# Kernel optimization log

Measured on AMD Instinct MI355X. Metric: run time of the kernel, lower is better.

## Reference

```python
import jax, jax.numpy as jnp
import numpy as np

FRAC_BIT = 12
SCALE = float(2 ** FRAC_BIT)          # 12 fractional bits
QMIN, QMAX = -32768.0, 32767.0        # signed 16-bit two's complement range


def quant16(x):
    """Quantize to signed 16-bit fixed point with 12 fractional bits.

    Matches float_to_16bits_tensor / bit_slice semantics: the bit-serial
    crossbar MVM of the sliced operands equals an exact integer product of
    these fixed-point values, rescaled back to float.
    """
    return jnp.clip(jnp.round(x * SCALE), QMIN, QMAX) / SCALE


def setup_inputs() -> dict:
    key = jax.random.key(0)
    k1, k2 = jax.random.split(key)
    x = jax.random.normal(k1, (32, 128, 56, 56), dtype=jnp.float32)
    # kaiming-ish scale so weights are well inside the fixed-point range
    weight = jax.random.normal(k2, (256, 128, 3, 3), dtype=jnp.float32) * 0.05
    return {"x": x, "weight": weight}


def reference(x, weight):
    # The nested i/j loop in the original slides a stride-1 window over the
    # zero-padded input, performing a bit-sliced crossbar MVM per pixel.
    # That is exactly conv2d(stride=1, padding=1) on 16-bit fixed-point
    # quantized input and weight (bias row in the crossbar is zero / unused).
    qx = quant16(x)
    qw = quant16(weight)
    out = jax.lax.conv_general_dilated(
        qx, qw,
        window_strides=(1, 1),
        padding=((1, 1), (1, 1)),
        dimension_numbers=("NCHW", "OIHW", "NCHW"),
    )
    return out
```

## Files before the change

### kernel.cpp

```cpp
#include <hip/hip_runtime.h>
#include <cstdint>
#include <cstddef>


typedef __attribute__((ext_vector_type(8))) short short8;
typedef __attribute__((ext_vector_type(4))) float floatx4;

#define NIMG 32
#define CIN  128
#define HW   56
#define KOUT 256
#define HP   58
#define XPAD_ELEMS ((size_t)NIMG * HP * HP * CIN)
#define WT_OFF_BYTES (XPAD_ELEMS * 2)
#define KK 1152

__device__ __forceinline__ uint16_t quant_bf16(float v) {
    float q = rintf(v * 4096.0f);
    q = fminf(fmaxf(q, -32768.0f), 32767.0f) * (1.0f / 4096.0f);
    union { float f; uint32_t u; } cv; cv.f = q;
    uint32_t u = cv.u;
    return (uint16_t)((u + 0x7fffu + ((u >> 16) & 1u)) >> 16);
}

__global__ __launch_bounds__(256) void quant_pad_x(const float* __restrict__ x,
                                                   uint16_t* __restrict__ xp) {
    const int b = blockIdx.x;
    const int n = b / HP, hp = b - n * HP;
    uint16_t* row = xp + (size_t)(n * HP + hp) * HP * CIN;

    if (hp == 0 || hp == HP - 1) {
        uint4 z{0, 0, 0, 0};
        uint4* d = (uint4*)row;
        for (int t = threadIdx.x; t < HP * CIN * 2 / 16; t += 256) d[t] = z;
        return;
    }
    const int h = hp - 1;
    __shared__ uint16_t tile[HW * 130];
    const float* src = x + (size_t)n * CIN * HW * HW + (size_t)h * HW;
    for (int t = threadIdx.x; t < CIN * 14; t += 256) {
        int c = t / 14, w4 = t - c * 14;
        float4 v = *(const float4*)(src + (size_t)c * (HW * HW) + w4 * 4);
        int base = (w4 * 4) * 130 + c;
        tile[base]       = quant_bf16(v.x);
        tile[base + 130] = quant_bf16(v.y);
        tile[base + 260] = quant_bf16(v.z);
        tile[base + 390] = quant_bf16(v.w);
    }
    __syncthreads();
    if (threadIdx.x < 32) {
        uint4 z{0, 0, 0, 0};
        if (threadIdx.x < 16) ((uint4*)row)[threadIdx.x] = z;
        else ((uint4*)(row + 57 * CIN))[threadIdx.x - 16] = z;
    }
    uint2* dst = (uint2*)(row + CIN);
    for (int t = threadIdx.x; t < (HW * CIN) / 4; t += 256) {
        int w = t >> 5, c4 = (t & 31) * 4;
        uint32_t a = tile[w * 130 + c4]     | ((uint32_t)tile[w * 130 + c4 + 1] << 16);
        uint32_t c = tile[w * 130 + c4 + 2] | ((uint32_t)tile[w * 130 + c4 + 3] << 16);
        dst[t] = make_uint2(a, c);
    }
}

__global__ __launch_bounds__(256) void quant_w(const float* __restrict__ w,
                                               uint16_t* __restrict__ wt) {
    int i = blockIdx.x * 256 + threadIdx.x;
    int k = i / KK;
    int r = i - k * KK;
    int tap = r >> 7;
    int c = r & 127;
    wt[i] = quant_bf16(w[(size_t)(k * CIN + c) * 9 + tap]);
}


#define GLOAD(gsrc, ldst)                                                      \
    __builtin_amdgcn_global_load_lds(                                          \
        (__attribute__((address_space(1))) void*)(void*)(gsrc),                \
        (__attribute__((address_space(3))) void*)(void*)(ldst), 16, 0, 0)

#define STAGE_A(bsel, kt) do {                                                 \
    GLOAD(aGp[0][0] + (size_t)(kt) * 64, &ldsA[bsel][0][(wv * 8) * 64]);       \
    GLOAD(aGp[0][1] + (size_t)(kt) * 64, &ldsA[bsel][0][(64 + wv * 8) * 64]);  \
    GLOAD(aGp[1][0] + (size_t)(kt) * 64, &ldsA[bsel][1][(wv * 8) * 64]);       \
    GLOAD(aGp[1][1] + (size_t)(kt) * 64, &ldsA[bsel][1][(64 + wv * 8) * 64]);  \
} while (0)

#define STAGE_B(bsel, kt) do {                                                 \
    const int tap_ = (kt) >> 1;                                                \
    const size_t boff_ = (size_t)((tap_ / 3) * HP + (tap_ % 3)) * CIN          \
                       + (size_t)((kt) & 1) * 64;                              \
    GLOAD(bGp[0][0] + boff_, &ldsB[bsel][0][(wv * 8) * 64]);                   \
    GLOAD(bGp[0][1] + boff_, &ldsB[bsel][0][(64 + wv * 8) * 64]);              \
    GLOAD(bGp[1][0] + boff_, &ldsB[bsel][1][(wv * 8) * 64]);                   \
    GLOAD(bGp[1][1] + boff_, &ldsB[bsel][1][(64 + wv * 8) * 64]);              \
} while (0)

#define READ_A(bsel, q4) do {                                                  \
    _Pragma("unroll")                                                          \
    for (int f_ = 0; f_ < 4; ++f_) {                                           \
        const int r_ = (q4) * 64 + f_ * 16 + m16;                              \
        ra[f_][0] = *(const short8*)&ldsA[bsel][wm][r_ * 64 + sl0];            \
        ra[f_][1] = *(const short8*)&ldsA[bsel][wm][r_ * 64 + sl1];            \
    }                                                                          \
} while (0)

#define READ_B(dst, bsel, ch) do {                                             \
    _Pragma("unroll")                                                          \
    for (int fc_ = 0; fc_ < 2; ++fc_) {                                        \
        const int r_ = bl + (ch) * 32 + fc_ * 16 + m16;                        \
        dst[fc_][0] = *(const short8*)&ldsB[bsel][bh][r_ * 64 + sl0];          \
        dst[fc_][1] = *(const short8*)&ldsB[bsel][bh][r_ * 64 + sl1];          \
    }                                                                          \
} while (0)

#define MFMA_Q(q4, ch, B) do {                                                 \
    _Pragma("unroll")                                                          \
    for (int s_ = 0; s_ < 2; ++s_)                                             \
    _Pragma("unroll")                                                          \
    for (int f_ = 0; f_ < 4; ++f_)                                             \
    _Pragma("unroll")                                                          \
    for (int c_ = 0; c_ < 2; ++c_)                                             \
        acc[q4][f_][ch][c_] = __builtin_amdgcn_mfma_f32_16x16x32_bf16(         \
            ra[f_][s_], B[c_][s_], acc[q4][f_][ch][c_], 0, 0, 0);              \
} while (0)

#define PHASE_TAIL(...) do {                                                   \
    __builtin_amdgcn_s_barrier();                                              \
    asm volatile("s_waitcnt lgkmcnt(0)" ::: "memory");                         \
    __builtin_amdgcn_s_setprio(1);                                             \
    __VA_ARGS__;                                                               \
    __builtin_amdgcn_s_setprio(0);                                             \
    __builtin_amdgcn_s_barrier();                                              \
} while (0)

__global__ __launch_bounds__(512, 2) void conv_gemm(const uint16_t* __restrict__ xp,
                                                    const uint16_t* __restrict__ wt,
                                                    float* __restrict__ out) {
    __shared__ __align__(16) uint16_t ldsA[2][2][128 * 64];
    __shared__ __align__(16) uint16_t ldsB[2][2][128 * 64];

    const int tid  = threadIdx.x;
    const int l    = tid & 63;
    const int wv   = tid >> 6;
    const int wm   = wv >> 2;
    const int wn   = wv & 3;
    const int bh   = wn >> 1;
    const int bl   = (wn & 1) * 64;
    const int srow = l >> 3;
    const int c_data = (l & 7) ^ srow;
    const int m16  = l & 15;
    const int q    = l >> 4;
    const int r7   = m16 & 7;
    const int sl0  = ((0 + q) ^ r7) * 8;
    const int sl1  = ((4 + q) ^ r7) * 8;

    const int b = blockIdx.x;
    const int pxblk = (b & 7) * 49 + (b >> 3);

    const uint16_t* aGp[2][2];
    const uint16_t* bGp[2][2];
#pragma unroll
    for (int h_ = 0; h_ < 2; ++h_)
#pragma unroll
        for (int j_ = 0; j_ < 2; ++j_) {
            const int row = h_ * 128 + j_ * 64 + wv * 8 + srow;
            aGp[h_][j_] = wt + (size_t)row * KK + c_data * 8;
            const int p = pxblk * 256 + row;
            const int n = p / 3136; const int rem = p - n * 3136;
            const int hh = rem / HW; const int ww = rem - hh * HW;
            bGp[h_][j_] = xp + (size_t)((n * HP + hh) * HP + ww) * CIN + c_data * 8;
        }

    floatx4 acc[2][4][2][2];
#pragma unroll
    for (int a_ = 0; a_ < 2; ++a_)
#pragma unroll
        for (int f_ = 0; f_ < 4; ++f_)
#pragma unroll
            for (int c_ = 0; c_ < 2; ++c_)
#pragma unroll
                for (int d_ = 0; d_ < 2; ++d_)
                    acc[a_][f_][c_][d_] = (floatx4){0.f, 0.f, 0.f, 0.f};

    short8 ra[4][2];
    short8 rb0[2][2];
    short8 rb1[2][2];

    STAGE_A(0, 0); STAGE_B(0, 0);
    STAGE_A(1, 1); STAGE_B(1, 1);
    asm volatile("s_waitcnt vmcnt(8)" ::: "memory");
    __builtin_amdgcn_s_barrier();

#pragma unroll 1
    for (int it = 0; it < 8; ++it) {
        const int ktE = 2 * it + 2;
        const int ktO = 2 * it + 3;
        READ_A(0, 0);
        READ_B(rb0, 0, 0);
        PHASE_TAIL(MFMA_Q(0, 0, rb0));
        READ_B(rb1, 0, 1);
        PHASE_TAIL(MFMA_Q(0, 1, rb1));
        READ_A(0, 1);
        PHASE_TAIL(MFMA_Q(1, 0, rb0));
        STAGE_A(0, ktE); STAGE_B(0, ktE);
        asm volatile("s_waitcnt vmcnt(8)" ::: "memory");
        PHASE_TAIL(MFMA_Q(1, 1, rb1));
        READ_A(1, 0);
        READ_B(rb0, 1, 0);
        PHASE_TAIL(MFMA_Q(0, 0, rb0));
        READ_B(rb1, 1, 1);
        PHASE_TAIL(MFMA_Q(0, 1, rb1));
        READ_A(1, 1);
        PHASE_TAIL(MFMA_Q(1, 0, rb0));
        STAGE_A(1, ktO); STAGE_B(1, ktO);
        asm volatile("s_waitcnt vmcnt(8)" ::: "memory");
        PHASE_TAIL(MFMA_Q(1, 1, rb1));
    }

    READ_A(0, 0);
    READ_B(rb0, 0, 0);
    PHASE_TAIL(MFMA_Q(0, 0, rb0));
    READ_B(rb1, 0, 1);
    PHASE_TAIL(MFMA_Q(0, 1, rb1));
    READ_A(0, 1);
    PHASE_TAIL(MFMA_Q(1, 0, rb0));
    asm volatile("s_waitcnt vmcnt(0)" ::: "memory");
    PHASE_TAIL(MFMA_Q(1, 1, rb1));
    READ_A(1, 0);
    READ_B(rb0, 1, 0);
    PHASE_TAIL(MFMA_Q(0, 0, rb0));
    READ_B(rb1, 1, 1);
    PHASE_TAIL(MFMA_Q(0, 1, rb1));
    READ_A(1, 1);
    PHASE_TAIL(MFMA_Q(1, 0, rb0));
    PHASE_TAIL(MFMA_Q(1, 1, rb1));

#pragma unroll
    for (int ch = 0; ch < 2; ++ch) {
        const int p0 = pxblk * 256 + wn * 64 + ch * 32 + m16;
        const int n = p0 / 3136; const int rem0 = p0 - n * 3136;
        float* opb = out + (size_t)(n * KOUT + wm * 128) * 3136 + rem0;
#pragma unroll
        for (int q4 = 0; q4 < 2; ++q4)
#pragma unroll
            for (int f = 0; f < 4; ++f) {
                const int kl = q4 * 64 + f * 16 + q * 4;
#pragma unroll
                for (int t = 0; t < 4; ++t) {
                    float* op = opb + (size_t)(kl + t) * 3136;
                    op[0]  = acc[q4][f][ch][0][t];
                    op[16] = acc[q4][f][ch][1][t];
                }
            }
    }
}

extern "C" void kernel_launch(void* const* d_in, const int* in_sizes, int n_in,
                              void* d_out, int out_size, void* d_ws, size_t ws_size,
                              hipStream_t stream) {
    const float* x = (const float*)d_in[0];
    const float* w = (const float*)d_in[1];
    float* out = (float*)d_out;

    uint16_t* xp  = (uint16_t*)d_ws;
    uint16_t* wtb = (uint16_t*)((char*)d_ws + WT_OFF_BYTES);

    quant_pad_x<<<NIMG * HP, 256, 0, stream>>>(x, xp);
    quant_w<<<(KOUT * KK) / 256, 256, 0, stream>>>(w, wtb);

    conv_gemm<<<dim3(392), dim3(512), 0, stream>>>(xp, wtb, out);
}
```

Before: 217.7 us.

## Cut per-phase barriers to two per k-tile in conv GEMM main loop

Replaces the eight barrier-pair phases per iteration with one body per k-tile that reads A/B fragments and issues MFMAs with no intermediate barriers, followed by a single barrier-stage-wait-barrier block. The goal is to remove frequent workgroup barriers and explicit lgkmcnt waits that serialize the waves and stall the MFMA pipe. The trade-off is that the compiler now places LDS waits itself, and the loss of lockstep wave interleaving may raise LDS contention or register pressure.

```diff
diff --git a/kernel.cpp b/kernel.cpp
--- a/kernel.cpp
+++ b/kernel.cpp
@@ -124,12 +124,25 @@
             ra[f_][s_], B[c_][s_], acc[q4][f_][ch][c_], 0, 0, 0);              \
 } while (0)
 
-#define PHASE_TAIL(...) do {                                                   \
+#define KT_BODY(bsel) do {                                                     \
+    READ_A(bsel, 0);                                                           \
+    READ_B(rb0, bsel, 0);                                                      \
+    READ_B(rb1, bsel, 1);                                                      \
+    __builtin_amdgcn_s_setprio(1);                                             \
+    MFMA_Q(0, 0, rb0);                                                         \
+    MFMA_Q(0, 1, rb1);                                                         \
+    __builtin_amdgcn_s_setprio(0);                                             \
+    READ_A(bsel, 1);                   \
+    __builtin_amdgcn_s_setprio(1);                                             \
+    MFMA_Q(1, 0, rb0);                                                         \
+    MFMA_Q(1, 1, rb1);                                                         \
+    __builtin_amdgcn_s_setprio(0);                                             \
+} while (0)
+
+#define KT_SYNC_STAGE(bsel, ktn) do {                                          \
     __builtin_amdgcn_s_barrier();                                              \
-    asm volatile("s_waitcnt lgkmcnt(0)" ::: "memory");                         \
-    __builtin_amdgcn_s_setprio(1);                                             \
-    __VA_ARGS__;                                                               \
-    __builtin_amdgcn_s_setprio(0);                                             \
+    STAGE_A(bsel, ktn); STAGE_B(bsel, ktn);                                    \
+    asm volatile("s_waitcnt vmcnt(8)" ::: "memory");                           \
     __builtin_amdgcn_s_barrier();                                              \
 } while (0)
 
@@ -195,45 +208,17 @@
     for (int it = 0; it < 8; ++it) {
         const int ktE = 2 * it + 2;
         const int ktO = 2 * it + 3;
-        READ_A(0, 0);
-        READ_B(rb0, 0, 0);
-        PHASE_TAIL(MFMA_Q(0, 0, rb0));
-        READ_B(rb1, 0, 1);
-        PHASE_TAIL(MFMA_Q(0, 1, rb1));
-        READ_A(0, 1);
-        PHASE_TAIL(MFMA_Q(1, 0, rb0));
-        STAGE_A(0, ktE); STAGE_B(0, ktE);
-        asm volatile("s_waitcnt vmcnt(8)" ::: "memory");
-        PHASE_TAIL(MFMA_Q(1, 1, rb1));
-        READ_A(1, 0);
-        READ_B(rb0, 1, 0);
-        PHASE_TAIL(MFMA_Q(0, 0, rb0));
-        READ_B(rb1, 1, 1);
-        PHASE_TAIL(MFMA_Q(0, 1, rb1));
-        READ_A(1, 1);
-        PHASE_TAIL(MFMA_Q(1, 0, rb0));
-        STAGE_A(1, ktO); STAGE_B(1, ktO);
-        asm volatile("s_waitcnt vmcnt(8)" ::: "memory");
-        PHASE_TAIL(MFMA_Q(1, 1, rb1));
-    }
-
-    READ_A(0, 0);
-    READ_B(rb0, 0, 0);
-    PHASE_TAIL(MFMA_Q(0, 0, rb0));
-    READ_B(rb1, 0, 1);
-    PHASE_TAIL(MFMA_Q(0, 1, rb1));
-    READ_A(0, 1);
-    PHASE_TAIL(MFMA_Q(1, 0, rb0));
+        KT_BODY(0);
+        KT_SYNC_STAGE(0, ktE);
+        KT_BODY(1);
+        KT_SYNC_STAGE(1, ktO);
+    }
+
+    KT_BODY(0);
+    __builtin_amdgcn_s_barrier();
     asm volatile("s_waitcnt vmcnt(0)" ::: "memory");
-    PHASE_TAIL(MFMA_Q(1, 1, rb1));
-    READ_A(1, 0);
-    READ_B(rb0, 1, 0);
-    PHASE_TAIL(MFMA_Q(0, 0, rb0));
-    READ_B(rb1, 1, 1);
-    PHASE_TAIL(MFMA_Q(0, 1, rb1));
-    READ_A(1, 1);
-    PHASE_TAIL(MFMA_Q(1, 0, rb0));
-    PHASE_TAIL(MFMA_Q(1, 1, rb1));
+    __builtin_amdgcn_s_barrier();
+    KT_BODY(1);
 
 #pragma unroll
     for (int ch = 0; ch < 2; ++ch) {
```

Result: faster. 212.7 us (-2.3%).
